# Optimization experiments

Hardware: AMD Instinct MI355X
Metric: run time of the kernel (lower is better)

Reference implementation:

```python
import jax, jax.numpy as jnp
import numpy as np

L = 3        # num_layers
H = 512      # hidden_dim
T = 64       # traj_len
LAT = 128    # latent_dim
COND = 128   # condition_dim
B = 2048     # batch


def setup_inputs() -> dict:
    key = jax.random.key(0)
    ks = jax.random.split(key, 8)
    s = 0.05
    d = LAT + COND
    return {
        "z": jax.random.normal(ks[0], (B, LAT), dtype=jnp.float32),
        "condition": jax.random.normal(ks[1], (B, COND), dtype=jnp.float32),
        # hidden_proj: Linear(latent+cond -> L*H)
        "hp_W": jax.random.normal(ks[2], (L * H, d), dtype=jnp.float32) * s,
        "hp_b": jnp.zeros((L * H,), dtype=jnp.float32),
        # GRU weights (PyTorch layout, gate order r,z,n)
        "W_ih0": jax.random.normal(ks[3], (3 * H, 2), dtype=jnp.float32) * s,
        "W_ih_rest": jax.random.normal(ks[4], (L - 1, 3 * H, H), dtype=jnp.float32) * s,
        "W_hh": jax.random.normal(ks[5], (L, 3 * H, H), dtype=jnp.float32) * s,
        "b_ih": jnp.zeros((L, 3 * H), dtype=jnp.float32),
        "b_hh": jnp.zeros((L, 3 * H), dtype=jnp.float32),
        # per-step output MLPs: Linear(H,H) -> ReLU -> Linear(H,2)
        "W1": jax.random.normal(ks[6], (T, H, H), dtype=jnp.float32) * s,
        "b1": jnp.zeros((T, H), dtype=jnp.float32),
        "W2": jax.random.normal(ks[7], (T, H, 2), dtype=jnp.float32) * s,
        "b2": jnp.zeros((T, 2), dtype=jnp.float32),
    }


def _gru_cell(x, h, W_ih, W_hh, b_ih, b_hh):
    # PyTorch GRU cell: gates in order (r, z, n)
    gi = x @ W_ih.T + b_ih        # (B, 3H)
    gh = h @ W_hh.T + b_hh        # (B, 3H)
    ir, iz, inn = jnp.split(gi, 3, axis=-1)
    hr, hz, hn = jnp.split(gh, 3, axis=-1)
    r = jax.nn.sigmoid(ir + hr)
    zg = jax.nn.sigmoid(iz + hz)
    n = jnp.tanh(inn + r * hn)
    return (1.0 - zg) * n + zg * h


def reference(z, condition, hp_W, hp_b, W_ih0, W_ih_rest, W_hh, b_ih, b_hh, W1, b1, W2, b2):
    Bsz = z.shape[0]
    combined = jnp.concatenate([z, condition], axis=1)            # (B, LAT+COND)
    h0 = (combined @ hp_W.T + hp_b).reshape(Bsz, L, H).transpose(1, 0, 2)  # (L, B, H)
    pos0 = jnp.zeros((Bsz, 2), dtype=z.dtype)

    def step(carry, ws):
        h, pos = carry                     # h: (L,B,H), pos: (B,2) = current_pos
        w1, bb1, w2, bb2 = ws              # this step's MLP weights
        x = pos
        new_h = []
        for l in range(L):                 # fixed small layer loop
            Wih = W_ih0 if l == 0 else W_ih_rest[l - 1]
            hl = _gru_cell(x, h[l], Wih, W_hh[l], b_ih[l], b_hh[l])
            new_h.append(hl)
            x = hl
        delta = jax.nn.relu(x @ w1 + bb1) @ w2 + bb2   # (B,2); dropout is identity at eval
        new_pos = pos + delta              # cumulative sum of deltas
        return (jnp.stack(new_h), new_pos), new_pos

    (_, _), traj = jax.lax.scan(step, (h0, pos0), (W1, b1, W2, b2))
    return traj.transpose(1, 0, 2)         # (B, T, 2)
```

## Files before the change

### kernel.cpp

```cpp
#include <hip/hip_runtime.h>
#include <hip/hip_bf16.h>


#define H 512
#define T_STEPS 64
#define BATCH 2048
#define H3 1536
#define D_IN 256
#define NSTRIP 8

typedef __bf16 bf16x8 __attribute__((ext_vector_type(8)));
typedef float f32x4 __attribute__((ext_vector_type(4)));
typedef unsigned short ushort8v __attribute__((ext_vector_type(8)));
typedef unsigned short ushort4v __attribute__((ext_vector_type(4)));

typedef const __attribute__((address_space(1))) unsigned int* gp1_t;
typedef __attribute__((address_space(3))) unsigned int* lp3_t;

__device__ inline void gload16(const unsigned short* g, unsigned short* l) {
    __builtin_amdgcn_global_load_lds((gp1_t)g, (lp3_t)l, 16, 0, 0);
}

__device__ inline unsigned short f2bf(float f) {
    union { float f; unsigned int u; } v{f};
    unsigned int r = v.u + 0x7fffu + ((v.u >> 16) & 1u);
    return (unsigned short)(r >> 16);
}
__device__ inline float bf2f(unsigned short u) {
    union { unsigned int u; float f; } v;
    v.u = ((unsigned int)u) << 16;
    return v.f;
}
__device__ inline float sigmoidf_(float x) { return 1.f / (1.f + expf(-x)); }

__device__ inline int soff64(int r, int kc) {
    return r * 64 + ((kc ^ (r & 7)) << 3);
}

__device__ inline void stage64(const unsigned short* src, int ld, int k0,
                               unsigned short* lds) {
    const int wid = threadIdx.x >> 6, lane = threadIdx.x & 63;
#pragma unroll
    for (int i = 0; i < 4; ++i) {
        int off = i * 4096 + wid * 1024 + lane * 16;
        int row = off >> 7;
        int c = (off >> 4) & 7;
        int cs = c ^ (row & 7);
        gload16(src + (size_t)row * ld + k0 + cs * 8,
                lds + ((i * 4096 + wid * 1024) >> 1));
    }
}

__device__ inline void gcore(const unsigned short* A0, int lda,
                             const unsigned short* W0, int K,
                             unsigned short (*As)[8192], unsigned short (*Ws)[8192],
                             f32x4 (&acc)[4][4]) {
    const int lane = threadIdx.x & 63, wid = threadIdx.x >> 6;
    const int wr = wid >> 1, wc = wid & 1;
    const int r16 = lane & 15, ko = lane >> 4;
#pragma unroll
    for (int i = 0; i < 4; ++i)
#pragma unroll
        for (int j = 0; j < 4; ++j) acc[i][j] = (f32x4)0.f;
    int aoff[2][4], boff[2][4];
#pragma unroll
    for (int kk = 0; kk < 2; ++kk)
#pragma unroll
        for (int i = 0; i < 4; ++i) {
            aoff[kk][i] = soff64(wr * 64 + i * 16 + r16, kk * 4 + ko);
            boff[kk][i] = soff64(wc * 64 + i * 16 + r16, kk * 4 + ko);
        }
    stage64(A0, lda, 0, As[0]);
    stage64(W0, K, 0, Ws[0]);
    __syncthreads();
    int cur = 0;
    for (int k0 = 0; k0 < K; k0 += 64) {
        const bool more = (k0 + 64) < K;
        if (more) {
            stage64(A0, lda, k0 + 64, As[cur ^ 1]);
            stage64(W0, K, k0 + 64, Ws[cur ^ 1]);
        }
#pragma unroll
        for (int kk = 0; kk < 2; ++kk) {
            bf16x8 a[4], b[4];
#pragma unroll
            for (int i = 0; i < 4; ++i) a[i] = *(const bf16x8*)&As[cur][aoff[kk][i]];
#pragma unroll
            for (int i = 0; i < 4; ++i) b[i] = *(const bf16x8*)&Ws[cur][boff[kk][i]];
#pragma unroll
            for (int mi = 0; mi < 4; ++mi)
#pragma unroll
                for (int ni = 0; ni < 4; ++ni)
                    acc[mi][ni] = __builtin_amdgcn_mfma_f32_16x16x32_bf16(
                        a[mi], b[ni], acc[mi][ni], 0, 0, 0);
        }
        if (more) {
            __syncthreads();
            cur ^= 1;
        }
    }
}

__device__ inline void epilogue_f32(f32x4 (&acc)[4][4], float* C, int ldc,
                                    const float* bias, unsigned short* Cbf,
                                    int brow, int bcol) {
    const int lane = threadIdx.x & 63, wid = threadIdx.x >> 6;
    const int wr = wid >> 1, wc = wid & 1, r16 = lane & 15;
    const int crow0 = brow + wr * 64 + (lane >> 4) * 4;
    const int ccol0 = bcol + wc * 64 + r16;
#pragma unroll
    for (int mi = 0; mi < 4; ++mi)
#pragma unroll
        for (int ni = 0; ni < 4; ++ni) {
            int col = ccol0 + ni * 16;
            float bv = bias ? bias[col] : 0.f;
#pragma unroll
            for (int j = 0; j < 4; ++j) {
                int row = crow0 + mi * 16 + j;
                float v = acc[mi][ni][j] + bv;
                C[(size_t)row * ldc + col] = v;
                if (Cbf) Cbf[(size_t)row * ldc + col] = f2bf(v);
            }
        }
}

__device__ inline void epilogue_bf(f32x4 (&acc)[4][4], unsigned short* C, int ldc,
                                   int brow, int bcol) {
    const int lane = threadIdx.x & 63, wid = threadIdx.x >> 6;
    const int wr = wid >> 1, wc = wid & 1, r16 = lane & 15;
    const int crow0 = brow + wr * 64 + (lane >> 4) * 4;
    const int ccol0 = bcol + wc * 64 + r16;
#pragma unroll
    for (int mi = 0; mi < 4; ++mi)
#pragma unroll
        for (int ni = 0; ni < 4; ++ni) {
            int col = ccol0 + ni * 16;
#pragma unroll
            for (int j = 0; j < 4; ++j) {
                int row = crow0 + mi * 16 + j;
                C[(size_t)row * ldc + col] = f2bf(acc[mi][ni][j]);
            }
        }
}

__device__ inline void epilogue_mlp(f32x4 (&acc)[4][4], const float* b1t,
                                    const float* W2t, float* partials, int brow,
                                    int bcol) {
    const int lane = threadIdx.x & 63, wid = threadIdx.x >> 6;
    const int wr = wid >> 1, wc = wid & 1, r16 = lane & 15;
    const int crow0 = brow + wr * 64 + (lane >> 4) * 4;
    const int ccol0 = bcol + wc * 64 + r16;
    const int strip = (bcol >> 7) * 2 + wc;
    float d0[4][4], d1[4][4];
#pragma unroll
    for (int mi = 0; mi < 4; ++mi)
#pragma unroll
        for (int j = 0; j < 4; ++j) { d0[mi][j] = 0.f; d1[mi][j] = 0.f; }
#pragma unroll
    for (int ni = 0; ni < 4; ++ni) {
        int col = ccol0 + ni * 16;
        float bv = b1t[col];
        float w20 = W2t[col * 2 + 0], w21 = W2t[col * 2 + 1];
#pragma unroll
        for (int mi = 0; mi < 4; ++mi)
#pragma unroll
            for (int j = 0; j < 4; ++j) {
                float hv = fmaxf(acc[mi][ni][j] + bv, 0.f);
                d0[mi][j] += hv * w20;
                d1[mi][j] += hv * w21;
            }
    }
#pragma unroll
    for (int m = 1; m < 16; m <<= 1)
#pragma unroll
        for (int mi = 0; mi < 4; ++mi)
#pragma unroll
            for (int j = 0; j < 4; ++j) {
                d0[mi][j] += __shfl_xor(d0[mi][j], m);
                d1[mi][j] += __shfl_xor(d1[mi][j], m);
            }
    if (r16 == 0) {
#pragma unroll
        for (int mi = 0; mi < 4; ++mi)
#pragma unroll
            for (int j = 0; j < 4; ++j) {
                int row = crow0 + mi * 16 + j;
                float2 v = make_float2(d0[mi][j], d1[mi][j]);
                *(float2*)&partials[((size_t)strip * BATCH + row) * 2] = v;
            }
    }
}

__global__ __launch_bounds__(256) void k_init(const unsigned short* comb,
                                              const unsigned short* hpW, float* h,
                                              unsigned short* h_bf,
                                              const float* hp_b) {
    __shared__ unsigned short As[2][8192], Ws[2][8192];
    f32x4 acc[4][4];
    int bid = blockIdx.x;
    int brow = (bid / 12) * 128, bcol = (bid % 12) * 128;
    gcore(comb + (size_t)brow * D_IN, D_IN, hpW + (size_t)bcol * D_IN, D_IN, As, Ws,
          acc);
    epilogue_f32(acc, h, H3, hp_b, h_bf, brow, bcol);
}

__global__ __launch_bounds__(256) void k_gh3(const unsigned short* h_bf,
                                             const unsigned short* Whh,
                                             unsigned short* gh0, unsigned short* gh1,
                                             unsigned short* gh2) {
    __shared__ unsigned short As[2][8192], Ws[2][8192];
    f32x4 acc[4][4];
    int bid = blockIdx.x;
    int g = bid / 192, r = bid % 192;
    int brow = (r / 12) * 128, bcol = (r % 12) * 128;
    unsigned short* C = (g == 0) ? gh0 : (g == 1 ? gh1 : gh2);
    gcore(h_bf + g * H + (size_t)brow * H3, H3,
          Whh + (size_t)g * H3 * H + (size_t)bcol * H, H, As, Ws, acc);
    epilogue_bf(acc, C, H3, brow, bcol);
}

__global__ __launch_bounds__(256) void k_dual(const unsigned short* A,
                                              const unsigned short* W0,
                                              unsigned short* C0,
                                              const unsigned short* W1,
                                              unsigned short* C1, int skip2) {
    __shared__ unsigned short As[2][8192], Ws[2][8192];
    f32x4 acc[4][4];
    int bid = blockIdx.x;
    int half = bid >= 192;
    if (half && skip2) return;
    int r = bid - half * 192;
    int brow = (r / 12) * 128, bcol = (r % 12) * 128;
    const unsigned short* W = half ? W1 : W0;
    unsigned short* C = half ? C1 : C0;
    gcore(A + (size_t)brow * H3, H3, W + (size_t)bcol * H, H, As, Ws, acc);
    epilogue_bf(acc, C, H3, brow, bcol);
}

__global__ __launch_bounds__(256) void k_mlp_gh(const unsigned short* A,
                                                const unsigned short* W1Tt,
                                                const float* b1t, const float* W2t,
                                                float* partials,
                                                const unsigned short* Whh2,
                                                unsigned short* gh2, int skip2) {
    __shared__ unsigned short As[2][8192], Ws[2][8192];
    f32x4 acc[4][4];
    int bid = blockIdx.x;
    if (bid < 64) {
        int brow = (bid >> 2) * 128, bcol = (bid & 3) * 128;
        gcore(A + (size_t)brow * H3, H3, W1Tt + (size_t)bcol * H, H, As, Ws, acc);
        epilogue_mlp(acc, b1t, W2t, partials, brow, bcol);
    } else {
        if (skip2) return;
        int r = bid - 64;
        int brow = (r / 12) * 128, bcol = (r % 12) * 128;
        gcore(A + (size_t)brow * H3, H3, Whh2 + (size_t)bcol * H, H, As, Ws, acc);
        epilogue_bf(acc, gh2, H3, brow, bcol);
    }
}

__global__ __launch_bounds__(256) void k_ew0(const unsigned short* gh0, float* h,
                                             unsigned short* h_bf,
                                             const float* W_ih0, const float* b_ih,
                                             const float* b_hh, float* pos,
                                             const float* partials, const float* b2,
                                             float* out, int t) {
    __shared__ float posS[2][2];
    const int tid = threadIdx.x, bid = blockIdx.x;
    if (tid < 2) {
        int b = bid * 2 + tid;
        float p0 = pos[b * 2 + 0], p1 = pos[b * 2 + 1];
        if (t > 0) {
            float s0 = 0.f, s1 = 0.f;
#pragma unroll
            for (int s = 0; s < NSTRIP; ++s) {
                float2 v = *(const float2*)&partials[((size_t)s * BATCH + b) * 2];
                s0 += v.x; s1 += v.y;
            }
            p0 += s0 + b2[(t - 1) * 2 + 0];
            p1 += s1 + b2[(t - 1) * 2 + 1];
            pos[b * 2 + 0] = p0;
            pos[b * 2 + 1] = p1;
            out[((size_t)b * T_STEPS + (t - 1)) * 2 + 0] = p0;
            out[((size_t)b * T_STEPS + (t - 1)) * 2 + 1] = p1;
        }
        posS[tid][0] = p0;
        posS[tid][1] = p1;
    }
    __syncthreads();
    const int lrow = tid >> 7, j0 = (tid & 127) * 4;
    const int b = bid * 2 + lrow;
    const size_t rb = (size_t)b * H3;
    const float px = posS[lrow][0], py = posS[lrow][1];
    ushort4v g0 = *(const ushort4v*)&gh0[rb + j0];
    ushort4v g1 = *(const ushort4v*)&gh0[rb + 512 + j0];
    ushort4v g2 = *(const ushort4v*)&gh0[rb + 1024 + j0];
    float4 h4 = *(const float4*)&h[rb + j0];
    float hv[4] = {h4.x, h4.y, h4.z, h4.w};
    float4 ho;
    ushort4v hbo;
#pragma unroll
    for (int k = 0; k < 4; ++k) {
        int j = j0 + k;
        float gi_r = px * W_ih0[j * 2 + 0] + py * W_ih0[j * 2 + 1] + b_ih[j];
        float gi_z = px * W_ih0[(512 + j) * 2 + 0] + py * W_ih0[(512 + j) * 2 + 1] +
                     b_ih[512 + j];
        float gi_n = px * W_ih0[(1024 + j) * 2 + 0] + py * W_ih0[(1024 + j) * 2 + 1] +
                     b_ih[1024 + j];
        float r = sigmoidf_(gi_r + bf2f(g0[k]) + b_hh[j]);
        float zg = sigmoidf_(gi_z + bf2f(g1[k]) + b_hh[512 + j]);
        float n = tanhf(gi_n + r * (bf2f(g2[k]) + b_hh[1024 + j]));
        float nh = (1.f - zg) * n + zg * hv[k];
        ((float*)&ho)[k] = nh;
        hbo[k] = f2bf(nh);
    }
    *(float4*)&h[rb + j0] = ho;
    *(ushort4v*)&h_bf[rb + j0] = hbo;
}

__global__ __launch_bounds__(256) void k_ewl(const unsigned short* gi,
                                             const unsigned short* gh, float* h,
                                             unsigned short* h_bf,
                                             const float* b_ihl, const float* b_hhl,
                                             int colOff) {
    const int tid = threadIdx.x, bid = blockIdx.x;
    const int lrow = tid >> 7, j0 = (tid & 127) * 4;
    const int b = bid * 2 + lrow;
    const size_t rb = (size_t)b * H3;
    ushort4v ir4 = *(const ushort4v*)&gi[rb + j0];
    ushort4v iz4 = *(const ushort4v*)&gi[rb + 512 + j0];
    ushort4v in4 = *(const ushort4v*)&gi[rb + 1024 + j0];
    ushort4v hr4 = *(const ushort4v*)&gh[rb + j0];
    ushort4v hz4 = *(const ushort4v*)&gh[rb + 512 + j0];
    ushort4v hn4 = *(const ushort4v*)&gh[rb + 1024 + j0];
    float4 bir = *(const float4*)&b_ihl[j0];
    float4 biz = *(const float4*)&b_ihl[512 + j0];
    float4 bin = *(const float4*)&b_ihl[1024 + j0];
    float4 bhr = *(const float4*)&b_hhl[j0];
    float4 bhz = *(const float4*)&b_hhl[512 + j0];
    float4 bhn = *(const float4*)&b_hhl[1024 + j0];
    float4 h4 = *(const float4*)&h[rb + colOff + j0];
    float bi_r[4] = {bir.x, bir.y, bir.z, bir.w};
    float bi_z[4] = {biz.x, biz.y, biz.z, biz.w};
    float bi_n[4] = {bin.x, bin.y, bin.z, bin.w};
    float bh_r[4] = {bhr.x, bhr.y, bhr.z, bhr.w};
    float bh_z[4] = {bhz.x, bhz.y, bhz.z, bhz.w};
    float bh_n[4] = {bhn.x, bhn.y, bhn.z, bhn.w};
    float hv[4] = {h4.x, h4.y, h4.z, h4.w};
    float4 ho;
    ushort4v hbo;
#pragma unroll
    for (int k = 0; k < 4; ++k) {
        float r = sigmoidf_(bf2f(ir4[k]) + bi_r[k] + bf2f(hr4[k]) + bh_r[k]);
        float zg = sigmoidf_(bf2f(iz4[k]) + bi_z[k] + bf2f(hz4[k]) + bh_z[k]);
        float n = tanhf(bf2f(in4[k]) + bi_n[k] + r * (bf2f(hn4[k]) + bh_n[k]));
        float nh = (1.f - zg) * n + zg * hv[k];
        ((float*)&ho)[k] = nh;
        hbo[k] = f2bf(nh);
    }
    *(float4*)&h[rb + colOff + j0] = ho;
    *(ushort4v*)&h_bf[rb + colOff + j0] = hbo;
}

__global__ __launch_bounds__(256) void k_posfin(const float* partials, float* pos,
                                                const float* b2, float* out) {
    int b = blockIdx.x * 256 + threadIdx.x;
    float s0 = 0.f, s1 = 0.f;
#pragma unroll
    for (int s = 0; s < NSTRIP; ++s) {
        float2 v = *(const float2*)&partials[((size_t)s * BATCH + b) * 2];
        s0 += v.x; s1 += v.y;
    }
    float p0 = pos[b * 2 + 0] + s0 + b2[63 * 2 + 0];
    float p1 = pos[b * 2 + 1] + s1 + b2[63 * 2 + 1];
    out[((size_t)b * T_STEPS + 63) * 2 + 0] = p0;
    out[((size_t)b * T_STEPS + 63) * 2 + 1] = p1;
}

__global__ __launch_bounds__(256) void k_comb(const float* z, const float* cond,
                                              unsigned short* comb, float* pos) {
    int idx = blockIdx.x * 256 + threadIdx.x;
    int b = idx >> 8, k = idx & 255;
    float v = (k < 128) ? z[b * 128 + k] : cond[b * 128 + (k - 128)];
    comb[idx] = f2bf(v);
    if (idx < BATCH * 2) pos[idx] = 0.f;
}

__global__ __launch_bounds__(256) void k_conv(const float* in, unsigned short* out) {
    size_t i = ((size_t)blockIdx.x * 256 + threadIdx.x) * 8;
    float4 v0 = *(const float4*)(in + i);
    float4 v1 = *(const float4*)(in + i + 4);
    ushort8v p;
    p[0] = f2bf(v0.x); p[1] = f2bf(v0.y); p[2] = f2bf(v0.z); p[3] = f2bf(v0.w);
    p[4] = f2bf(v1.x); p[5] = f2bf(v1.y); p[6] = f2bf(v1.z); p[7] = f2bf(v1.w);
    *(ushort8v*)(out + i) = p;
}

__global__ __launch_bounds__(256) void k_trw1(const float* W1, unsigned short* W1T) {
    __shared__ float tile[32][33];
    int t = blockIdx.z;
    int n0 = blockIdx.x * 32, k0 = blockIdx.y * 32;
    int tx = threadIdx.x & 31, ty = threadIdx.x >> 5;
#pragma unroll
    for (int j = 0; j < 4; ++j)
        tile[ty + 8 * j][tx] = W1[((size_t)t * 512 + k0 + ty + 8 * j) * 512 + n0 + tx];
    __syncthreads();
#pragma unroll
    for (int j = 0; j < 4; ++j)
        W1T[((size_t)t * 512 + n0 + ty + 8 * j) * 512 + k0 + tx] =
            f2bf(tile[tx][ty + 8 * j]);
}

extern "C" void kernel_launch(void* const* d_in, const int* in_sizes, int n_in,
                              void* d_out, int out_size, void* d_ws, size_t ws_size,
                              hipStream_t stream) {
    const float* z = (const float*)d_in[0];
    const float* cond = (const float*)d_in[1];
    const float* hp_W = (const float*)d_in[2];
    const float* hp_b = (const float*)d_in[3];
    const float* W_ih0 = (const float*)d_in[4];
    const float* W_ihr = (const float*)d_in[5];
    const float* W_hh = (const float*)d_in[6];
    const float* b_ih = (const float*)d_in[7];
    const float* b_hh = (const float*)d_in[8];
    const float* W1 = (const float*)d_in[9];
    const float* b1 = (const float*)d_in[10];
    const float* W2 = (const float*)d_in[11];
    const float* b2 = (const float*)d_in[12];
    float* out = (float*)d_out;

    char* w = (char*)d_ws;
    float* pos = (float*)w;           w += (size_t)BATCH * 2 * 4;
    float* partials = (float*)w;      w += (size_t)NSTRIP * BATCH * 2 * 4;
    float* h = (float*)w;             w += (size_t)BATCH * H3 * 4;
    unsigned short* gi = (unsigned short*)w;      w += (size_t)BATCH * H3 * 2;
    unsigned short* gh0 = (unsigned short*)w;     w += (size_t)BATCH * H3 * 2;
    unsigned short* gh1 = (unsigned short*)w;     w += (size_t)BATCH * H3 * 2;
    unsigned short* gh2 = (unsigned short*)w;     w += (size_t)BATCH * H3 * 2;
    unsigned short* h_bf = (unsigned short*)w;    w += (size_t)BATCH * H3 * 2;
    unsigned short* comb_bf = (unsigned short*)w; w += (size_t)BATCH * D_IN * 2;
    unsigned short* hpW_bf = (unsigned short*)w;  w += (size_t)H3 * D_IN * 2;
    unsigned short* Whh_bf = (unsigned short*)w;  w += (size_t)3 * H3 * H * 2;
    unsigned short* Wihr_bf = (unsigned short*)w; w += (size_t)2 * H3 * H * 2;
    unsigned short* W1T_bf = (unsigned short*)w;  w += (size_t)T_STEPS * H * H * 2;

    k_comb<<<dim3((BATCH * D_IN) / 256), dim3(256), 0, stream>>>(z, cond, comb_bf, pos);
    k_conv<<<dim3((H3 * D_IN) / 2048), dim3(256), 0, stream>>>(hp_W, hpW_bf);
    k_conv<<<dim3((3 * H3 * H) / 2048), dim3(256), 0, stream>>>(W_hh, Whh_bf);
    k_conv<<<dim3((2 * H3 * H) / 2048), dim3(256), 0, stream>>>(W_ihr, Wihr_bf);
    k_trw1<<<dim3(16, 16, T_STEPS), dim3(256), 0, stream>>>(W1, W1T_bf);
    k_init<<<dim3(192), dim3(256), 0, stream>>>(comb_bf, hpW_bf, h, h_bf, hp_b);
    k_gh3<<<dim3(576), dim3(256), 0, stream>>>(h_bf, Whh_bf, gh0, gh1, gh2);

    for (int t = 0; t < T_STEPS; ++t) {
        int last = (t == T_STEPS - 1) ? 1 : 0;
        k_ew0<<<dim3(1024), dim3(256), 0, stream>>>(gh0, h, h_bf, W_ih0, b_ih, b_hh,
                                                    pos, partials, b2, out, t);
        k_dual<<<dim3(384), dim3(256), 0, stream>>>(h_bf, Wihr_bf, gi, Whh_bf, gh0,
                                                    last);
        k_ewl<<<dim3(1024), dim3(256), 0, stream>>>(gi, gh1, h, h_bf, b_ih + H3,
                                                    b_hh + H3, H);
        k_dual<<<dim3(384), dim3(256), 0, stream>>>(
            h_bf + H, Wihr_bf + (size_t)H3 * H, gi, Whh_bf + (size_t)H3 * H, gh1,
            last);
        k_ewl<<<dim3(1024), dim3(256), 0, stream>>>(gi, gh2, h, h_bf, b_ih + 2 * H3,
                                                    b_hh + 2 * H3, 2 * H);
        k_mlp_gh<<<dim3(256), dim3(256), 0, stream>>>(
            h_bf + 2 * H, W1T_bf + (size_t)t * H * H, b1 + (size_t)t * H,
            W2 + (size_t)t * H * 2, partials, Whh_bf + (size_t)2 * H3 * H, gh2, last);
    }
    k_posfin<<<dim3(8), dim3(256), 0, stream>>>(partials, pos, b2, out);
}
```

Measured before the change: 3.850 ms.

## Fuse GRU input-gate GEMM with gate elementwise update in a single kernel

Replaces the per-layer pair of a dual GEMM kernel plus a separate elementwise GRU kernel with one fused kernel. Its gi blocks compute all three gate columns (r, z, n) for a 128x64 tile, then apply the GRU update directly from an LDS transpose. The remaining blocks compute the next step's hidden-hidden GEMM as before. This removes the bf16 gi buffer round trip through global memory and two launches per timestep. In exchange, the gi tiles are smaller, the K step is 32 with more barriers, and the fused kernel uses more registers for three gate accumulators.

```diff
diff --git a/kernel.cpp b/kernel.cpp
--- a/kernel.cpp
+++ b/kernel.cpp
@@ -36,7 +36,6 @@
 __device__ inline int soff64(int r, int kc) {
     return r * 64 + ((kc ^ (r & 7)) << 3);
 }
-
 __device__ inline void stage64(const unsigned short* src, int ld, int k0,
                                unsigned short* lds) {
     const int wid = threadIdx.x >> 6, lane = threadIdx.x & 63;
@@ -50,11 +49,11 @@
                 lds + ((i * 4096 + wid * 1024) >> 1));
     }
 }
-
-__device__ inline void gcore(const unsigned short* A0, int lda,
-                             const unsigned short* W0, int K,
-                             unsigned short (*As)[8192], unsigned short (*Ws)[8192],
-                             f32x4 (&acc)[4][4]) {
+__device__ inline void gcore64(const unsigned short* A0, int lda,
+                               const unsigned short* W0, int K,
+                               unsigned short* As0, unsigned short* As1,
+                               unsigned short* Ws0, unsigned short* Ws1,
+                               f32x4 (&acc)[4][4]) {
     const int lane = threadIdx.x & 63, wid = threadIdx.x >> 6;
     const int wr = wid >> 1, wc = wid & 1;
     const int r16 = lane & 15, ko = lane >> 4;
@@ -70,23 +69,25 @@
             aoff[kk][i] = soff64(wr * 64 + i * 16 + r16, kk * 4 + ko);
             boff[kk][i] = soff64(wc * 64 + i * 16 + r16, kk * 4 + ko);
         }
-    stage64(A0, lda, 0, As[0]);
-    stage64(W0, K, 0, Ws[0]);
+    stage64(A0, lda, 0, As0);
+    stage64(W0, K, 0, Ws0);
     __syncthreads();
     int cur = 0;
     for (int k0 = 0; k0 < K; k0 += 64) {
         const bool more = (k0 + 64) < K;
         if (more) {
-            stage64(A0, lda, k0 + 64, As[cur ^ 1]);
-            stage64(W0, K, k0 + 64, Ws[cur ^ 1]);
-        }
+            stage64(A0, lda, k0 + 64, cur ? As0 : As1);
+            stage64(W0, K, k0 + 64, cur ? Ws0 : Ws1);
+        }
+        const unsigned short* Ac = cur ? As1 : As0;
+        const unsigned short* Wc = cur ? Ws1 : Ws0;
 #pragma unroll
         for (int kk = 0; kk < 2; ++kk) {
             bf16x8 a[4], b[4];
 #pragma unroll
-            for (int i = 0; i < 4; ++i) a[i] = *(const bf16x8*)&As[cur][aoff[kk][i]];
-#pragma unroll
-            for (int i = 0; i < 4; ++i) b[i] = *(const bf16x8*)&Ws[cur][boff[kk][i]];
+            for (int i = 0; i < 4; ++i) a[i] = *(const bf16x8*)&Ac[aoff[kk][i]];
+#pragma unroll
+            for (int i = 0; i < 4; ++i) b[i] = *(const bf16x8*)&Wc[boff[kk][i]];
 #pragma unroll
             for (int mi = 0; mi < 4; ++mi)
 #pragma unroll
@@ -99,6 +100,32 @@
             cur ^= 1;
         }
     }
+}
+
+__device__ inline int soff32(int r, int kc) {
+    return r * 32 + ((kc ^ ((r >> 1) & 3)) << 3);
+}
+__device__ inline void stage32a(const unsigned short* src, int ld, int k0,
+                                unsigned short* lds) {
+    const int wid = threadIdx.x >> 6, lane = threadIdx.x & 63;
+#pragma unroll
+    for (int i = 0; i < 2; ++i) {
+        int off = i * 4096 + wid * 1024 + lane * 16;
+        int row = off >> 6;
+        int c = (off >> 4) & 3;
+        int cs = c ^ ((row >> 1) & 3);
+        gload16(src + (size_t)row * ld + k0 + cs * 8,
+                lds + ((i * 4096 + wid * 1024) >> 1));
+    }
+}
+__device__ inline void stage32w(const unsigned short* src, int ld, int k0,
+                                unsigned short* lds) {
+    const int wid = threadIdx.x >> 6, lane = threadIdx.x & 63;
+    int off = wid * 1024 + lane * 16;
+    int row = off >> 6;
+    int c = (off >> 4) & 3;
+    int cs = c ^ ((row >> 1) & 3);
+    gload16(src + (size_t)row * ld + k0 + cs * 8, lds + ((wid * 1024) >> 1));
 }
 
 __device__ inline void epilogue_f32(f32x4 (&acc)[4][4], float* C, int ldc,
@@ -191,6 +218,148 @@
     }
 }
 
+__global__ __launch_bounds__(256) void k_fused(
+    const unsigned short* A, const unsigned short* Wih, const unsigned short* ghIn,
+    const float* bi, const float* bh, float* h, unsigned short* h_bf, int colOff,
+    const unsigned short* Whh, unsigned short* ghOut, int skip2) {
+    __shared__ __attribute__((aligned(16))) char shraw[65536];
+    const int bid = blockIdx.x;
+    const int lane = threadIdx.x & 63, wid = threadIdx.x >> 6;
+    const int wr = wid >> 1, wc = wid & 1;
+    const int r16 = lane & 15, ko = lane >> 4;
+
+    if (bid >= 128) {
+        if (skip2) return;
+        int r = bid - 128;
+        int brow = (r / 12) * 128, bcol = (r % 12) * 128;
+        f32x4 acc[4][4];
+        gcore64(A + (size_t)brow * H3, H3, Whh + (size_t)bcol * H, H,
+                (unsigned short*)shraw, (unsigned short*)(shraw + 16384),
+                (unsigned short*)(shraw + 32768),
+                (unsigned short*)(shraw + 49152), acc);
+        epilogue_bf(acc, ghOut, H3, brow, bcol);
+        return;
+    }
+
+    const int brow = (bid >> 3) * 128, bcol = (bid & 7) * 64;
+    unsigned short* As0 = (unsigned short*)shraw;
+    unsigned short* As1 = (unsigned short*)(shraw + 8192);
+    unsigned short* Ws0 = (unsigned short*)(shraw + 16384);
+    unsigned short* Ws1 = (unsigned short*)(shraw + 28672);
+    float* ldsT = (float*)shraw;
+
+    f32x4 acc[3][4][2];
+#pragma unroll
+    for (int g = 0; g < 3; ++g)
+#pragma unroll
+        for (int mi = 0; mi < 4; ++mi)
+#pragma unroll
+            for (int ni = 0; ni < 2; ++ni) acc[g][mi][ni] = (f32x4)0.f;
+    int aoff[4], boff[2];
+#pragma unroll
+    for (int mi = 0; mi < 4; ++mi) aoff[mi] = soff32(wr * 64 + mi * 16 + r16, ko);
+#pragma unroll
+    for (int ni = 0; ni < 2; ++ni) boff[ni] = soff32(wc * 32 + ni * 16 + r16, ko);
+
+    const unsigned short* A0 = A + (size_t)brow * H3;
+    stage32a(A0, H3, 0, As0);
+#pragma unroll
+    for (int g = 0; g < 3; ++g)
+        stage32w(Wih + (size_t)(g * 512 + bcol) * 512, 512, 0, Ws0 + g * 2048);
+    __syncthreads();
+    int cur = 0;
+    for (int k0 = 0; k0 < 512; k0 += 32) {
+        const bool more = (k0 + 32) < 512;
+        if (more) {
+            stage32a(A0, H3, k0 + 32, cur ? As0 : As1);
+#pragma unroll
+            for (int g = 0; g < 3; ++g)
+                stage32w(Wih + (size_t)(g * 512 + bcol) * 512, 512, k0 + 32,
+                         (cur ? Ws0 : Ws1) + g * 2048);
+        }
+        const unsigned short* Ac = cur ? As1 : As0;
+        const unsigned short* Wc = cur ? Ws1 : Ws0;
+        bf16x8 a[4];
+#pragma unroll
+        for (int mi = 0; mi < 4; ++mi) a[mi] = *(const bf16x8*)&Ac[aoff[mi]];
+#pragma unroll
+        for (int g = 0; g < 3; ++g) {
+            bf16x8 b0 = *(const bf16x8*)&Wc[g * 2048 + boff[0]];
+            bf16x8 b1 = *(const bf16x8*)&Wc[g * 2048 + boff[1]];
+#pragma unroll
+            for (int mi = 0; mi < 4; ++mi) {
+                acc[g][mi][0] = __builtin_amdgcn_mfma_f32_16x16x32_bf16(
+                    a[mi], b0, acc[g][mi][0], 0, 0, 0);
+                acc[g][mi][1] = __builtin_amdgcn_mfma_f32_16x16x32_bf16(
+                    a[mi], b1, acc[g][mi][1], 0, 0, 0);
+            }
+        }
+        if (more) {
+            __syncthreads();
+            cur ^= 1;
+        }
+    }
+
+    const int row_rd = threadIdx.x >> 1;
+    const int half = threadIdx.x & 1;
+    const int c0 = half * 16;
+#pragma unroll
+    for (int ni = 0; ni < 2; ++ni) {
+        __syncthreads();
+#pragma unroll
+        for (int g = 0; g < 3; ++g)
+#pragma unroll
+            for (int mi = 0; mi < 4; ++mi)
+#pragma unroll
+                for (int j = 0; j < 4; ++j) {
+                    int rw = wr * 64 + mi * 16 + (lane >> 4) * 4 + j;
+                    ldsT[((g << 7) + rw) * 33 + wc * 16 + r16] = acc[g][mi][ni][j];
+                }
+        __syncthreads();
+        const int gcol0 = bcol + half * 32 + ni * 16;
+        const int b = brow + row_rd;
+        const size_t rb = (size_t)b * H3;
+#pragma unroll
+        for (int q = 0; q < 4; ++q) {
+            int gc = gcol0 + q * 4;
+            float4 biR = *(const float4*)&bi[gc];
+            float4 biZ = *(const float4*)&bi[512 + gc];
+            float4 biN = *(const float4*)&bi[1024 + gc];
+            float4 bhR = *(const float4*)&bh[gc];
+            float4 bhZ = *(const float4*)&bh[512 + gc];
+            float4 bhN = *(const float4*)&bh[1024 + gc];
+            ushort4v gR = *(const ushort4v*)&ghIn[rb + gc];
+            ushort4v gZ = *(const ushort4v*)&ghIn[rb + 512 + gc];
+            ushort4v gN = *(const ushort4v*)&ghIn[rb + 1024 + gc];
+            float4 hOld = *(const float4*)&h[rb + colOff + gc];
+            float biRv[4] = {biR.x, biR.y, biR.z, biR.w};
+            float biZv[4] = {biZ.x, biZ.y, biZ.z, biZ.w};
+            float biNv[4] = {biN.x, biN.y, biN.z, biN.w};
+            float bhRv[4] = {bhR.x, bhR.y, bhR.z, bhR.w};
+            float bhZv[4] = {bhZ.x, bhZ.y, bhZ.z, bhZ.w};
+            float bhNv[4] = {bhN.x, bhN.y, bhN.z, bhN.w};
+            float hOv[4] = {hOld.x, hOld.y, hOld.z, hOld.w};
+            float4 hNew;
+            ushort4v hNb;
+#pragma unroll
+            for (int k = 0; k < 4; ++k) {
+                int c = c0 + q * 4 + k;
+                float ra = ldsT[(0 * 128 + row_rd) * 33 + c];
+                float za = ldsT[(1 * 128 + row_rd) * 33 + c];
+                float na = ldsT[(2 * 128 + row_rd) * 33 + c];
+                float r_ = sigmoidf_(ra + biRv[k] + bf2f(gR[k]) + bhRv[k]);
+                float z_ = sigmoidf_(za + biZv[k] + bf2f(gZ[k]) + bhZv[k]);
+                float n_ = tanhf(na + biNv[k] + r_ * (bf2f(gN[k]) + bhNv[k]));
+                float nh = (1.f - z_) * n_ + z_ * hOv[k];
+                ((float*)&hNew)[k] = nh;
+                hNb[k] = f2bf(nh);
+            }
+            *(float4*)&h[rb + colOff + gc] = hNew;
+            *(ushort4v*)&h_bf[rb + colOff + gc] = hNb;
+        }
+    }
+}
+
 __global__ __launch_bounds__(256) void k_init(const unsigned short* comb,
                                               const unsigned short* hpW, float* h,
                                               unsigned short* h_bf,
@@ -199,8 +368,8 @@
     f32x4 acc[4][4];
     int bid = blockIdx.x;
     int brow = (bid / 12) * 128, bcol = (bid % 12) * 128;
-    gcore(comb + (size_t)brow * D_IN, D_IN, hpW + (size_t)bcol * D_IN, D_IN, As, Ws,
-          acc);
+    gcore64(comb + (size_t)brow * D_IN, D_IN, hpW + (size_t)bcol * D_IN, D_IN,
+            As[0], As[1], Ws[0], Ws[1], acc);
     epilogue_f32(acc, h, H3, hp_b, h_bf, brow, bcol);
 }
 
@@ -214,26 +383,9 @@
     int g = bid / 192, r = bid % 192;
     int brow = (r / 12) * 128, bcol = (r % 12) * 128;
     unsigned short* C = (g == 0) ? gh0 : (g == 1 ? gh1 : gh2);
-    gcore(h_bf + g * H + (size_t)brow * H3, H3,
-          Whh + (size_t)g * H3 * H + (size_t)bcol * H, H, As, Ws, acc);
-    epilogue_bf(acc, C, H3, brow, bcol);
-}
-
-__global__ __launch_bounds__(256) void k_dual(const unsigned short* A,
-                                              const unsigned short* W0,
-                                              unsigned short* C0,
-                                              const unsigned short* W1,
-                                              unsigned short* C1, int skip2) {
-    __shared__ unsigned short As[2][8192], Ws[2][8192];
-    f32x4 acc[4][4];
-    int bid = blockIdx.x;
-    int half = bid >= 192;
-    if (half && skip2) return;
-    int r = bid - half * 192;
-    int brow = (r / 12) * 128, bcol = (r % 12) * 128;
-    const unsigned short* W = half ? W1 : W0;
-    unsigned short* C = half ? C1 : C0;
-    gcore(A + (size_t)brow * H3, H3, W + (size_t)bcol * H, H, As, Ws, acc);
+    gcore64(h_bf + g * H + (size_t)brow * H3, H3,
+            Whh + (size_t)g * H3 * H + (size_t)bcol * H, H, As[0], As[1], Ws[0],
+            Ws[1], acc);
     epilogue_bf(acc, C, H3, brow, bcol);
 }
 
@@ -248,13 +400,15 @@
     int bid = blockIdx.x;
     if (bid < 64) {
         int brow = (bid >> 2) * 128, bcol = (bid & 3) * 128;
-        gcore(A + (size_t)brow * H3, H3, W1Tt + (size_t)bcol * H, H, As, Ws, acc);
+        gcore64(A + (size_t)brow * H3, H3, W1Tt + (size_t)bcol * H, H, As[0],
+                As[1], Ws[0], Ws[1], acc);
         epilogue_mlp(acc, b1t, W2t, partials, brow, bcol);
     } else {
         if (skip2) return;
         int r = bid - 64;
         int brow = (r / 12) * 128, bcol = (r % 12) * 128;
-        gcore(A + (size_t)brow * H3, H3, Whh2 + (size_t)bcol * H, H, As, Ws, acc);
+        gcore64(A + (size_t)brow * H3, H3, Whh2 + (size_t)bcol * H, H, As[0],
+                As[1], Ws[0], Ws[1], acc);
         epilogue_bf(acc, gh2, H3, brow, bcol);
     }
 }
@@ -316,50 +470,6 @@
     }
     *(float4*)&h[rb + j0] = ho;
     *(ushort4v*)&h_bf[rb + j0] = hbo;
-}
-
-__global__ __launch_bounds__(256) void k_ewl(const unsigned short* gi,
-                                             const unsigned short* gh, float* h,
-                                             unsigned short* h_bf,
-                                             const float* b_ihl, const float* b_hhl,
-                                             int colOff) {
-    const int tid = threadIdx.x, bid = blockIdx.x;
-    const int lrow = tid >> 7, j0 = (tid & 127) * 4;
-    const int b = bid * 2 + lrow;
-    const size_t rb = (size_t)b * H3;
-    ushort4v ir4 = *(const ushort4v*)&gi[rb + j0];
-    ushort4v iz4 = *(const ushort4v*)&gi[rb + 512 + j0];
-    ushort4v in4 = *(const ushort4v*)&gi[rb + 1024 + j0];
-    ushort4v hr4 = *(const ushort4v*)&gh[rb + j0];
-    ushort4v hz4 = *(const ushort4v*)&gh[rb + 512 + j0];
-    ushort4v hn4 = *(const ushort4v*)&gh[rb + 1024 + j0];
-    float4 bir = *(const float4*)&b_ihl[j0];
-    float4 biz = *(const float4*)&b_ihl[512 + j0];
-    float4 bin = *(const float4*)&b_ihl[1024 + j0];
-    float4 bhr = *(const float4*)&b_hhl[j0];
-    float4 bhz = *(const float4*)&b_hhl[512 + j0];
-    float4 bhn = *(const float4*)&b_hhl[1024 + j0];
-    float4 h4 = *(const float4*)&h[rb + colOff + j0];
-    float bi_r[4] = {bir.x, bir.y, bir.z, bir.w};
-    float bi_z[4] = {biz.x, biz.y, biz.z, biz.w};
-    float bi_n[4] = {bin.x, bin.y, bin.z, bin.w};
-    float bh_r[4] = {bhr.x, bhr.y, bhr.z, bhr.w};
-    float bh_z[4] = {bhz.x, bhz.y, bhz.z, bhz.w};
-    float bh_n[4] = {bhn.x, bhn.y, bhn.z, bhn.w};
-    float hv[4] = {h4.x, h4.y, h4.z, h4.w};
-    float4 ho;
-    ushort4v hbo;
-#pragma unroll
-    for (int k = 0; k < 4; ++k) {
-        float r = sigmoidf_(bf2f(ir4[k]) + bi_r[k] + bf2f(hr4[k]) + bh_r[k]);
-        float zg = sigmoidf_(bf2f(iz4[k]) + bi_z[k] + bf2f(hz4[k]) + bh_z[k]);
-        float n = tanhf(bf2f(in4[k]) + bi_n[k] + r * (bf2f(hn4[k]) + bh_n[k]));
-        float nh = (1.f - zg) * n + zg * hv[k];
-        ((float*)&ho)[k] = nh;
-        hbo[k] = f2bf(nh);
-    }
-    *(float4*)&h[rb + colOff + j0] = ho;
-    *(ushort4v*)&h_bf[rb + colOff + j0] = hbo;
 }
 
 __global__ __launch_bounds__(256) void k_posfin(const float* partials, float* pos,
@@ -433,7 +543,6 @@
     float* pos = (float*)w;           w += (size_t)BATCH * 2 * 4;
     float* partials = (float*)w;      w += (size_t)NSTRIP * BATCH * 2 * 4;
     float* h = (float*)w;             w += (size_t)BATCH * H3 * 4;
-    unsigned short* gi = (unsigned short*)w;      w += (size_t)BATCH * H3 * 2;
     unsigned short* gh0 = (unsigned short*)w;     w += (size_t)BATCH * H3 * 2;
     unsigned short* gh1 = (unsigned short*)w;     w += (size_t)BATCH * H3 * 2;
     unsigned short* gh2 = (unsigned short*)w;     w += (size_t)BATCH * H3 * 2;
@@ -452,22 +561,24 @@
     k_init<<<dim3(192), dim3(256), 0, stream>>>(comb_bf, hpW_bf, h, h_bf, hp_b);
     k_gh3<<<dim3(576), dim3(256), 0, stream>>>(h_bf, Whh_bf, gh0, gh1, gh2);
 
+    const unsigned short* Whh0 = Whh_bf;
+    const unsigned short* Whh1 = Whh_bf + (size_t)H3 * H;
+    const unsigned short* Whh2 = Whh_bf + (size_t)2 * H3 * H;
+    const unsigned short* Wihr0 = Wihr_bf;
+    const unsigned short* Wihr1 = Wihr_bf + (size_t)H3 * H;
+
     for (int t = 0; t < T_STEPS; ++t) {
         int last = (t == T_STEPS - 1) ? 1 : 0;
         k_ew0<<<dim3(1024), dim3(256), 0, stream>>>(gh0, h, h_bf, W_ih0, b_ih, b_hh,
                                                     pos, partials, b2, out, t);
-        k_dual<<<dim3(384), dim3(256), 0, stream>>>(h_bf, Wihr_bf, gi, Whh_bf, gh0,
-                                                    last);
-        k_ewl<<<dim3(1024), dim3(256), 0, stream>>>(gi, gh1, h, h_bf, b_ih + H3,
-                                                    b_hh + H3, H);
-        k_dual<<<dim3(384), dim3(256), 0, stream>>>(
-            h_bf + H, Wihr_bf + (size_t)H3 * H, gi, Whh_bf + (size_t)H3 * H, gh1,
-            last);
-        k_ewl<<<dim3(1024), dim3(256), 0, stream>>>(gi, gh2, h, h_bf, b_ih + 2 * H3,
-                                                    b_hh + 2 * H3, 2 * H);
+        k_fused<<<dim3(320), dim3(256), 0, stream>>>(
+            h_bf, Wihr0, gh1, b_ih + H3, b_hh + H3, h, h_bf, H, Whh0, gh0, last);
+        k_fused<<<dim3(320), dim3(256), 0, stream>>>(
+            h_bf + H, Wihr1, gh2, b_ih + 2 * H3, b_hh + 2 * H3, h, h_bf, 2 * H,
+            Whh1, gh1, last);
         k_mlp_gh<<<dim3(256), dim3(256), 0, stream>>>(
             h_bf + 2 * H, W1T_bf + (size_t)t * H * H, b1 + (size_t)t * H,
-            W2 + (size_t)t * H * 2, partials, Whh_bf + (size_t)2 * H3 * H, gh2, last);
+            W2 + (size_t)t * H * 2, partials, Whh2, gh2, last);
     }
     k_posfin<<<dim3(8), dim3(256), 0, stream>>>(partials, pos, b2, out);
 }
```

Result: slower. 5.264 ms (+36.7%).
